# Optimization experiments

Hardware: AMD Instinct MI355X
Metric: run time of the kernel (lower is better)

## Reference

```python
import jax, jax.numpy as jnp
import numpy as np

HEADS1, HID, LSTM_H, OUT = 4, 64, 32, 2
NEG_SLOPE = 0.2
EPS = 1e-16


def gat_layer(x, src, dst, W, att_src, att_dst, bias, heads, out_ch):
    """PyG GATConv (concat=True, add_self_loops handled by caller)."""
    N = x.shape[0]
    h = (x @ W).reshape(N, heads, out_ch)                 # [N, H, C]
    a_s = jnp.sum(h * att_src, axis=-1)                    # [N, H]
    a_d = jnp.sum(h * att_dst, axis=-1)                    # [N, H]
    e = jax.nn.leaky_relu(a_s[src] + a_d[dst], NEG_SLOPE)  # [E, H]
    m = jax.ops.segment_max(e, dst, num_segments=N)        # scatter-softmax (stable)
    e = jnp.exp(e - jax.lax.stop_gradient(m)[dst])
    denom = jax.ops.segment_sum(e, dst, num_segments=N)
    alpha = e / (denom[dst] + EPS)                         # [E, H]
    msg = h[src] * alpha[..., None]                        # [E, H, C]
    out = jax.ops.segment_sum(msg, dst, num_segments=N)    # [N, H, C]
    return out.reshape(N, heads * out_ch) + bias


def lstm_last(seq, W_ih, W_hh, b_ih, b_hh, hidden):
    """Single-layer batch_first LSTM; returns last-step hidden state. Gate order i,f,g,o (torch)."""
    B = seq.shape[0]
    xT = jnp.transpose(seq, (1, 0, 2))  # [T, B, F]
    b = b_ih + b_hh

    def step(carry, xt):
        h, c = carry
        z = xt @ W_ih.T + h @ W_hh.T + b  # [B, 4H]
        i, f, g, o = jnp.split(z, 4, axis=-1)
        c = jax.nn.sigmoid(f) * c + jax.nn.sigmoid(i) * jnp.tanh(g)
        h = jax.nn.sigmoid(o) * jnp.tanh(c)
        return (h, c), None

    h0 = jnp.zeros((B, hidden), seq.dtype)
    (h, _), _ = jax.lax.scan(step, (h0, h0), xT)
    return h


def setup_inputs() -> dict:
    key = jax.random.key(0)
    ks = jax.random.split(key, 20)
    N, E, IN, T = 50000, 800000, 128, 50
    s = lambda k, shp: jax.random.normal(k, shp, jnp.float32) * 0.05
    inp = {
        "x": jax.random.normal(ks[0], (N, IN), jnp.float32),
        "edge_index": jax.random.randint(ks[1], (2, E), 0, N, jnp.int32),
        "sequences": jax.random.normal(ks[2], (N, T, 3), jnp.float32),
        # GATConv 1: in=128 -> 64 per head, 4 heads
        "W1": s(ks[3], (IN, HEADS1 * HID)),
        "att_src1": s(ks[4], (HEADS1, HID)),
        "att_dst1": s(ks[5], (HEADS1, HID)),
        "bias1": jnp.zeros((HEADS1 * HID,), jnp.float32),
        # GATConv 2: in=256 -> 64, 1 head
        "W2": s(ks[6], (HEADS1 * HID, HID)),
        "att_src2": s(ks[7], (1, HID)),
        "att_dst2": s(ks[8], (1, HID)),
        "bias2": jnp.zeros((HID,), jnp.float32),
        # LSTM(input_size=3, hidden_size=32)
        "W_ih": s(ks[9], (4 * LSTM_H, 3)),
        "W_hh": s(ks[10], (4 * LSTM_H, LSTM_H)),
        "b_ih": jnp.zeros((4 * LSTM_H,), jnp.float32),
        "b_hh": jnp.zeros((4 * LSTM_H,), jnp.float32),
        # fusion MLP: (64+32) -> 64 -> 2
        "Wf1": s(ks[11], (HID + LSTM_H, HID)),
        "bf1": jnp.zeros((HID,), jnp.float32),
        "Wf2": s(ks[12], (HID, OUT)),
        "bf2": jnp.zeros((OUT,), jnp.float32),
    }
    return inp


def reference(x, edge_index, sequences, W1, att_src1, att_dst1, bias1,
              W2, att_src2, att_dst2, bias2, W_ih, W_hh, b_ih, b_hh,
              Wf1, bf1, Wf2, bf2):
    N = x.shape[0]
    # PyG GATConv default add_self_loops=True
    loops = jnp.arange(N, dtype=edge_index.dtype)
    src = jnp.concatenate([edge_index[0], loops])
    dst = jnp.concatenate([edge_index[1], loops])

    g = jax.nn.elu(gat_layer(x, src, dst, W1, att_src1, att_dst1, bias1, HEADS1, HID))
    # dropout is identity in eval mode
    g = gat_layer(g, src, dst, W2, att_src2, att_dst2, bias2, 1, HID)  # [N, 64]

    t = lstm_last(sequences, W_ih, W_hh, b_ih, b_hh, LSTM_H)           # [N, 32]

    combined = jnp.concatenate([g, t], axis=1)
    h = jax.nn.relu(combined @ Wf1 + bf1)
    return h @ Wf2 + bf2
```

## Files before the change

### kernel.cpp

```cpp
#include <hip/hip_runtime.h>
#include <math.h>

#define HEADS1 4
#define HID 64
#define LSTM_H 32
#define IN_F 128
#define T_STEPS 50
#define NEG_SLOPE 0.2f
#define EPS_A 1e-16f

typedef __attribute__((ext_vector_type(8))) short short8;
typedef __attribute__((ext_vector_type(4))) float floatx4;
typedef __attribute__((ext_vector_type(4))) unsigned uint32x4;

__device__ __forceinline__ float frcp(float x) {
    float r;
    asm("v_rcp_f32 %0, %1" : "=v"(r) : "v"(x));
    return r;
}
__device__ __forceinline__ float sigf(float x) { return frcp(1.0f + __expf(-x)); }
__device__ __forceinline__ float tanhfast(float x) {
    float e = __expf(2.0f * x);
    return 1.0f - 2.0f * frcp(e + 1.0f);
}
__device__ __forceinline__ unsigned short f2bf(float f) {
    unsigned u = __float_as_uint(f);
    unsigned r = (u + 0x7FFFu + ((u >> 16) & 1u)) >> 16;
    return (unsigned short)r;
}
__device__ __forceinline__ float bf2f(unsigned short s) {
    return __uint_as_float(((unsigned)s) << 16);
}
__device__ __forceinline__ unsigned cvt_pk_bf16(float a, float b) {
    unsigned r;
    asm("v_cvt_pk_bf16_f32 %0, %1, %2" : "=v"(r) : "v"(a), "v"(b));
    return r;
}
__device__ __forceinline__ float lo16f(unsigned p) { return __uint_as_float(p << 16); }
__device__ __forceinline__ float hi16f(unsigned p) { return __uint_as_float(p & 0xffff0000u); }
__device__ __forceinline__ short8 bc8(uint32x4 v) { return __builtin_bit_cast(short8, v); }

template <int KK>
__global__ void prep_wt(const float* __restrict__ W, unsigned short* __restrict__ th,
                        unsigned short* __restrict__ tl, int total, int NC) {
    int i = blockIdx.x * 256 + threadIdx.x;
    if (i >= total) return;
    int n = i / KK, k = i - n * KK;
    float v = W[k * NC + n];
    unsigned short h = f2bf(v);
    th[i] = h;
    tl[i] = f2bf(v - bf2f(h));
}

template <int K, int NC>
__global__ __launch_bounds__(256)
void gemm_mfma(const float* __restrict__ A, const unsigned short* __restrict__ Bth,
               const unsigned short* __restrict__ Btl, float* __restrict__ C, int M) {
    __shared__ float sA[128][44];
    __shared__ unsigned short sBh[64][40];
    __shared__ unsigned short sBl[64][40];
    const int tid = threadIdx.x;
    const int wave = tid >> 6, lane = tid & 63;
    const int wr = wave >> 1, wc = wave & 1;
    const int row0 = blockIdx.x * 128;
    const int col0 = blockIdx.y * 64;
    const int l15 = lane & 15, l4 = lane >> 4;

    floatx4 acc[4][2];
#pragma unroll
    for (int rb = 0; rb < 4; rb++)
#pragma unroll
        for (int cb = 0; cb < 2; cb++) acc[rb][cb] = (floatx4){0.f, 0.f, 0.f, 0.f};

    for (int k0 = 0; k0 < K; k0 += 32) {
        __syncthreads();
#pragma unroll
        for (int q = 0; q < 4; q++) {
            int idx = q * 256 + tid;
            int row = idx >> 3, seg = idx & 7;
            int gr = row0 + row;
            float4 v = (gr < M) ? *(const float4*)&A[(size_t)gr * K + k0 + seg * 4]
                                : make_float4(0.f, 0.f, 0.f, 0.f);
            *(float4*)&sA[row][seg * 4] = v;
        }
        {
            int col = tid >> 2, seg = tid & 3;
            size_t gb = (size_t)(col0 + col) * K + k0 + seg * 8;
            *(short8*)&sBh[col][seg * 8] = *(const short8*)&Bth[gb];
            *(short8*)&sBl[col][seg * 8] = *(const short8*)&Btl[gb];
        }
        __syncthreads();

        short8 bh0 = *(const short8*)&sBh[wc * 32 + 0 + l15][l4 * 8];
        short8 bl0 = *(const short8*)&sBl[wc * 32 + 0 + l15][l4 * 8];
        short8 bh1 = *(const short8*)&sBh[wc * 32 + 16 + l15][l4 * 8];
        short8 bl1 = *(const short8*)&sBl[wc * 32 + 16 + l15][l4 * 8];

#pragma unroll
        for (int rb = 0; rb < 4; rb++) {
            int row = wr * 64 + rb * 16 + l15;
            floatx4 a0 = *(const floatx4*)&sA[row][l4 * 8 + 0];
            floatx4 a1 = *(const floatx4*)&sA[row][l4 * 8 + 4];
            unsigned p0 = cvt_pk_bf16(a0[0], a0[1]);
            unsigned p1 = cvt_pk_bf16(a0[2], a0[3]);
            unsigned p2 = cvt_pk_bf16(a1[0], a1[1]);
            unsigned p3 = cvt_pk_bf16(a1[2], a1[3]);
            uint32x4 hp = {p0, p1, p2, p3};
            short8 Ah = bc8(hp);
            unsigned q0 = cvt_pk_bf16(a0[0] - lo16f(p0), a0[1] - hi16f(p0));
            unsigned q1 = cvt_pk_bf16(a0[2] - lo16f(p1), a0[3] - hi16f(p1));
            unsigned q2 = cvt_pk_bf16(a1[0] - lo16f(p2), a1[1] - hi16f(p2));
            unsigned q3 = cvt_pk_bf16(a1[2] - lo16f(p3), a1[3] - hi16f(p3));
            uint32x4 lp = {q0, q1, q2, q3};
            short8 Al = bc8(lp);

            acc[rb][0] = __builtin_amdgcn_mfma_f32_16x16x32_bf16(Ah, bh0, acc[rb][0], 0, 0, 0);
            acc[rb][0] = __builtin_amdgcn_mfma_f32_16x16x32_bf16(Ah, bl0, acc[rb][0], 0, 0, 0);
            acc[rb][0] = __builtin_amdgcn_mfma_f32_16x16x32_bf16(Al, bh0, acc[rb][0], 0, 0, 0);
            acc[rb][1] = __builtin_amdgcn_mfma_f32_16x16x32_bf16(Ah, bh1, acc[rb][1], 0, 0, 0);
            acc[rb][1] = __builtin_amdgcn_mfma_f32_16x16x32_bf16(Ah, bl1, acc[rb][1], 0, 0, 0);
            acc[rb][1] = __builtin_amdgcn_mfma_f32_16x16x32_bf16(Al, bh1, acc[rb][1], 0, 0, 0);
        }
    }

#pragma unroll
    for (int rb = 0; rb < 4; rb++)
#pragma unroll
        for (int cb = 0; cb < 2; cb++)
#pragma unroll
            for (int q = 0; q < 4; q++) {
                int row = row0 + wr * 64 + rb * 16 + l4 * 4 + q;
                int col = col0 + wc * 32 + cb * 16 + l15;
                if (row < M) C[(size_t)row * NC + col] = acc[rb][cb][q];
            }
}

__global__ void att_scores(const float* __restrict__ h, const float* __restrict__ att_s,
                           const float* __restrict__ att_d, float* __restrict__ as_,
                           float* __restrict__ ad_, int NH, int Hmask) {
    int i = blockIdx.x * blockDim.x + threadIdx.x;
    if (i >= NH) return;
    int hh = i & Hmask;
    const float* row = h + (size_t)i * HID;
    float s = 0.0f, d = 0.0f;
#pragma unroll 8
    for (int c = 0; c < HID; c++) {
        float v = row[c];
        s += v * att_s[hh * HID + c];
        d += v * att_d[hh * HID + c];
    }
    as_[i] = s;
    ad_[i] = d;
}

__global__ void count_deg(const int* __restrict__ dsts, int E, int ET, int* __restrict__ cnt) {
    int e = blockIdx.x * blockDim.x + threadIdx.x;
    if (e >= ET) return;
    int d = (e < E) ? dsts[e] : (e - E);
    atomicAdd(&cnt[d], 1);
}

__global__ void scan1(const int* __restrict__ cnt, int* __restrict__ rowp,
                      int* __restrict__ bsum, int N) {
    __shared__ int tmp[256];
    int i = blockIdx.x * 256 + threadIdx.x;
    int v = (i < N) ? cnt[i] : 0;
    tmp[threadIdx.x] = v;
    __syncthreads();
    for (int off = 1; off < 256; off <<= 1) {
        int t = (threadIdx.x >= (unsigned)off) ? tmp[threadIdx.x - off] : 0;
        __syncthreads();
        tmp[threadIdx.x] += t;
        __syncthreads();
    }
    if (i < N) rowp[i] = tmp[threadIdx.x] - v;
    if (threadIdx.x == 255) bsum[blockIdx.x] = tmp[255];
}

__global__ void scan2(int* __restrict__ bsum, int nb) {
    __shared__ int tmp[256];
    int v = (threadIdx.x < (unsigned)nb) ? bsum[threadIdx.x] : 0;
    tmp[threadIdx.x] = v;
    __syncthreads();
    for (int off = 1; off < 256; off <<= 1) {
        int t = (threadIdx.x >= (unsigned)off) ? tmp[threadIdx.x - off] : 0;
        __syncthreads();
        tmp[threadIdx.x] += t;
        __syncthreads();
    }
    if (threadIdx.x < (unsigned)nb) bsum[threadIdx.x] = tmp[threadIdx.x] - v;
}

__global__ void scan3(int* __restrict__ rowp, const int* __restrict__ bsum, int N, int ET) {
    int i = blockIdx.x * 256 + threadIdx.x;
    if (i < N) rowp[i] += bsum[blockIdx.x];
    if (i == 0) rowp[N] = ET;
}

__global__ void scatter_edges(const int* __restrict__ dsts, int E, int ET,
                              const int* __restrict__ rowp, int* __restrict__ cursor,
                              int* __restrict__ eid) {
    int e = blockIdx.x * blockDim.x + threadIdx.x;
    if (e >= ET) return;
    int d = (e < E) ? dsts[e] : (e - E);
    int pos = atomicAdd(&cursor[d], 1);
    eid[rowp[d] + pos] = e;
}

__global__ __launch_bounds__(256)
void gat_agg4_sp(const int* __restrict__ srcs, int E,
                 const int* __restrict__ rowp, const int* __restrict__ eid,
                 const float* __restrict__ as_, const float* __restrict__ ad_,
                 const float* __restrict__ hfeat, const float* __restrict__ bias,
                 float* __restrict__ g, int N) {
    __shared__ float s_alpha[4][64][4];
    const int wave = threadIdx.x >> 6;
    const int lane = threadIdx.x & 63;
    const int head = lane >> 4;
    const int dst = blockIdx.x * 4 + wave;
    if (dst >= N) return;
    const int start = rowp[dst], end = rowp[dst + 1];
    const float4 adv = ((const float4*)ad_)[dst];
    const float4* h4 = (const float4*)hfeat;

    float4 dsum = make_float4(0.f, 0.f, 0.f, 0.f);
    float4 acc  = make_float4(0.f, 0.f, 0.f, 0.f);

    for (int i0 = start; i0 < end; i0 += 64) {
        int cnt = min(64, end - i0);
        int i = i0 + lane;
        int s = 0;
        if (i < end) {
            int e = eid[i];
            s = (e < E) ? srcs[e] : (e - E);
            float4 a = ((const float4*)as_)[s];
            float tx, ex;
            tx = a.x + adv.x; tx = (tx > 0.f) ? tx : NEG_SLOPE * tx; ex = __expf(tx);
            dsum.x += ex; s_alpha[wave][lane][0] = ex;
            tx = a.y + adv.y; tx = (tx > 0.f) ? tx : NEG_SLOPE * tx; ex = __expf(tx);
            dsum.y += ex; s_alpha[wave][lane][1] = ex;
            tx = a.z + adv.z; tx = (tx > 0.f) ? tx : NEG_SLOPE * tx; ex = __expf(tx);
            dsum.z += ex; s_alpha[wave][lane][2] = ex;
            tx = a.w + adv.w; tx = (tx > 0.f) ? tx : NEG_SLOPE * tx; ex = __expf(tx);
            dsum.w += ex; s_alpha[wave][lane][3] = ex;
        }
        __builtin_amdgcn_wave_barrier();
#pragma unroll 4
        for (int k = 0; k < cnt; k++) {
            float a_k = s_alpha[wave][k][head];
            int   s_k = __shfl(s, k);
            float4 hv = h4[(size_t)s_k * 64 + lane];
            acc.x += a_k * hv.x; acc.y += a_k * hv.y;
            acc.z += a_k * hv.z; acc.w += a_k * hv.w;
        }
        __builtin_amdgcn_wave_barrier();
    }
#pragma unroll
    for (int mk = 32; mk >= 1; mk >>= 1) {
        dsum.x += __shfl_xor(dsum.x, mk);
        dsum.y += __shfl_xor(dsum.y, mk);
        dsum.z += __shfl_xor(dsum.z, mk);
        dsum.w += __shfl_xor(dsum.w, mk);
    }
    float den = (head == 0) ? dsum.x : (head == 1) ? dsum.y : (head == 2) ? dsum.z : dsum.w;
    float inv = 1.0f / (den + EPS_A);
    float4 b4 = ((const float4*)bias)[lane];
    float4 r;
    r.x = acc.x * inv + b4.x; r.x = (r.x > 0.f) ? r.x : __expf(r.x) - 1.f;
    r.y = acc.y * inv + b4.y; r.y = (r.y > 0.f) ? r.y : __expf(r.y) - 1.f;
    r.z = acc.z * inv + b4.z; r.z = (r.z > 0.f) ? r.z : __expf(r.z) - 1.f;
    r.w = acc.w * inv + b4.w; r.w = (r.w > 0.f) ? r.w : __expf(r.w) - 1.f;
    ((float4*)g)[(size_t)dst * 64 + lane] = r;
}

__global__ __launch_bounds__(256)
void gat_agg1_sp(const int* __restrict__ srcs, int E,
                 const int* __restrict__ rowp, const int* __restrict__ eid,
                 const float* __restrict__ as_, const float* __restrict__ ad_,
                 const float* __restrict__ hfeat, const float* __restrict__ bias,
                 float* __restrict__ g, int N) {
    __shared__ float s_alpha[4][64];
    const int wave = threadIdx.x >> 6;
    const int lane = threadIdx.x & 63;
    const int dst = blockIdx.x * 4 + wave;
    if (dst >= N) return;
    const int start = rowp[dst], end = rowp[dst + 1];
    const float adv = ad_[dst];

    float dsum = 0.0f, acc = 0.0f;
    for (int i0 = start; i0 < end; i0 += 64) {
        int cnt = min(64, end - i0);
        int i = i0 + lane;
        int s = 0;
        if (i < end) {
            int e = eid[i];
            s = (e < E) ? srcs[e] : (e - E);
            float t = as_[s] + adv;
            t = (t > 0.f) ? t : NEG_SLOPE * t;
            float ex = __expf(t);
            dsum += ex;
            s_alpha[wave][lane] = ex;
        }
        __builtin_amdgcn_wave_barrier();
#pragma unroll 4
        for (int k = 0; k < cnt; k++) {
            float a_k = s_alpha[wave][k];
            int   s_k = __shfl(s, k);
            acc += a_k * hfeat[(size_t)s_k * 64 + lane];
        }
        __builtin_amdgcn_wave_barrier();
    }
#pragma unroll
    for (int mk = 32; mk >= 1; mk >>= 1) dsum += __shfl_xor(dsum, mk);
    g[(size_t)dst * 64 + lane] = acc / (dsum + EPS_A) + bias[lane];
}

__global__ void prep_wsplit(const float* __restrict__ Wih, const float* __restrict__ Whh,
                            const float* __restrict__ bih, const float* __restrict__ bhh,
                            uint32x4* __restrict__ wsp) {
    const int tid = threadIdx.x;
    const int kk = tid >> 7, sub = (tid >> 6) & 1, lane = tid & 63;
    const int grp = lane >> 4, col = lane & 15;
    const int krow = grp * 8;
    const int n = (sub + kk * 2) * 16 + col;
    float w[8];
    *(float4*)&w[0] = *(const float4*)&Whh[n * 32 + krow + 0];
    *(float4*)&w[4] = *(const float4*)&Whh[n * 32 + krow + 4];
    unsigned hi[8], lo[8];
#pragma unroll
    for (int j = 0; j < 8; j++) {
        unsigned short hs = f2bf(w[j]);
        hi[j] = hs;
        lo[j] = f2bf(w[j] - bf2f(hs));
    }
    uint32x4 BH = {hi[0] | (hi[1] << 16), hi[2] | (hi[3] << 16),
                   hi[4] | (hi[5] << 16), hi[6] | (hi[7] << 16)};
    uint32x4 BL = {lo[0] | (lo[1] << 16), lo[2] | (lo[3] << 16),
                   lo[4] | (lo[5] << 16), lo[6] | (lo[7] << 16)};
    float wi0 = Wih[n * 3 + 0], wi1 = Wih[n * 3 + 1], wi2 = Wih[n * 3 + 2];
    float bb = bih[n] + bhh[n];
    unsigned h0 = f2bf(wi0), h1 = f2bf(wi1), h2 = f2bf(wi2), hb = f2bf(bb);
    uint32x4 B2 = {0u, 0u, 0u, 0u};
    if (grp == 0) {
        unsigned bl_ = f2bf(bb - bf2f((unsigned short)hb));
        B2[0] = h0 | (h1 << 16); B2[1] = h2 | (hb << 16);
        B2[2] = h0 | (h1 << 16); B2[3] = h2 | (bl_ << 16);
    } else if (grp == 1) {
        unsigned l0 = f2bf(wi0 - bf2f((unsigned short)h0));
        unsigned l1 = f2bf(wi1 - bf2f((unsigned short)h1));
        unsigned l2 = f2bf(wi2 - bf2f((unsigned short)h2));
        B2[0] = l0 | (l1 << 16); B2[1] = l2;
    }
    wsp[((kk * 3 + 0) * 2 + sub) * 64 + lane] = B2;
    wsp[((kk * 3 + 1) * 2 + sub) * 64 + lane] = BH;
    wsp[((kk * 3 + 2) * 2 + sub) * 64 + lane] = BL;
}

__global__ __launch_bounds__(256)
void lstm_mfma(const float* __restrict__ seq, const uint32x4* __restrict__ wsp,
               float* __restrict__ t_out, int N) {
    __shared__ float s_h[2][2][16][36];

    const int tid  = threadIdx.x;
    const int wave = tid >> 6, lane = tid & 63;
    const int pair = wave >> 1, sub = wave & 1;
    const int grp  = lane >> 4, col = lane & 15;
    const int node0 = blockIdx.x * 32 + pair * 16;

#define LF(KK, W) wsp[(((KK) * 3 + (W)) * 2 + sub) * 64 + lane]
    uint32x4 B2_0 = LF(0, 0), BH_0 = LF(0, 1), BL_0 = LF(0, 2);
    uint32x4 B2_1 = LF(1, 0), BH_1 = LF(1, 1), BL_1 = LF(1, 2);
    uint32x4 B2_2 = LF(2, 0), BH_2 = LF(2, 1), BL_2 = LF(2, 2);
    uint32x4 B2_3 = LF(3, 0), BH_3 = LF(3, 1), BL_3 = LF(3, 2);
#undef LF
    asm volatile("" : "+v"(B2_0), "+v"(BH_0), "+v"(BL_0),
                      "+v"(B2_1), "+v"(BH_1), "+v"(BL_1),
                      "+v"(B2_2), "+v"(BH_2), "+v"(BL_2),
                      "+v"(B2_3), "+v"(BH_3), "+v"(BL_3));

    for (int i = tid; i < 2 * 2 * 16 * 36; i += 256) ((float*)s_h)[i] = 0.0f;
    __syncthreads();

    float cst0 = 0.f, cst1 = 0.f, cst2 = 0.f, cst3 = 0.f;
    float hn0 = 0.f, hn1 = 0.f, hn2 = 0.f, hn3 = 0.f;
    const floatx4 zac = {0.f, 0.f, 0.f, 0.f};

    const int nodeX = node0 + col;
    const bool vx = (nodeX < N) && (grp < 2);
    const bool g0 = (grp == 0);
    const float* xp = seq + (size_t)nodeX * (T_STEPS * 3);

    float xv0 = vx ? xp[0] : 0.0f;
    float xv1 = vx ? xp[1] : 0.0f;
    float xv2 = vx ? xp[2] : 0.0f;

#pragma unroll 1
    for (int t = 0; t < T_STEPS; t++) {
        unsigned w0 = cvt_pk_bf16(xv0, xv1);
        unsigned w1 = cvt_pk_bf16(xv2, g0 ? 1.0f : 0.0f);
        float e0 = xv0 - lo16f(w0);
        float e1 = xv1 - hi16f(w0);
        float e2 = xv2 - lo16f(w1);
        unsigned w2 = g0 ? cvt_pk_bf16(e0, e1) : 0u;
        unsigned w3 = g0 ? cvt_pk_bf16(e2, 1.0f) : 0u;
        uint32x4 a2p = {w0, w1, w2, w3};
        short8 A2 = bc8(a2p);

        const float* hr = &s_h[pair][(t + 1) & 1][col][grp * 8];
        floatx4 h0 = *(const floatx4*)&hr[0];
        floatx4 h1 = *(const floatx4*)&hr[4];
        unsigned p0 = cvt_pk_bf16(h0[0], h0[1]);
        unsigned p1 = cvt_pk_bf16(h0[2], h0[3]);
        unsigned p2 = cvt_pk_bf16(h1[0], h1[1]);
        unsigned p3 = cvt_pk_bf16(h1[2], h1[3]);
        uint32x4 hip = {p0, p1, p2, p3};
        short8 Ahi = bc8(hip);
        unsigned q0 = cvt_pk_bf16(h0[0] - lo16f(p0), h0[1] - hi16f(p0));
        unsigned q1 = cvt_pk_bf16(h0[2] - lo16f(p1), h0[3] - hi16f(p1));
        unsigned q2 = cvt_pk_bf16(h1[0] - lo16f(p2), h1[1] - hi16f(p2));
        unsigned q3 = cvt_pk_bf16(h1[2] - lo16f(p3), h1[3] - hi16f(p3));
        uint32x4 lop = {q0, q1, q2, q3};
        short8 Alo = bc8(lop);

        {
            int tn = (t + 1 < T_STEPS) ? (t + 1) : t;
            xv0 = vx ? xp[tn * 3 + 0] : 0.0f;
            xv1 = vx ? xp[tn * 3 + 1] : 0.0f;
            xv2 = vx ? xp[tn * 3 + 2] : 0.0f;
        }

        floatx4 d0 = __builtin_amdgcn_mfma_f32_16x16x32_bf16(A2, bc8(B2_0), zac, 0, 0, 0);
        d0 = __builtin_amdgcn_mfma_f32_16x16x32_bf16(Alo, bc8(BH_0), d0, 0, 0, 0);
        d0 = __builtin_amdgcn_mfma_f32_16x16x32_bf16(Ahi, bc8(BL_0), d0, 0, 0, 0);
        d0 = __builtin_amdgcn_mfma_f32_16x16x32_bf16(Ahi, bc8(BH_0), d0, 0, 0, 0);
        floatx4 d1 = __builtin_amdgcn_mfma_f32_16x16x32_bf16(A2, bc8(B2_1), zac, 0, 0, 0);
        d1 = __builtin_amdgcn_mfma_f32_16x16x32_bf16(Alo, bc8(BH_1), d1, 0, 0, 0);
        d1 = __builtin_amdgcn_mfma_f32_16x16x32_bf16(Ahi, bc8(BL_1), d1, 0, 0, 0);
        d1 = __builtin_amdgcn_mfma_f32_16x16x32_bf16(Ahi, bc8(BH_1), d1, 0, 0, 0);
        floatx4 d2 = __builtin_amdgcn_mfma_f32_16x16x32_bf16(A2, bc8(B2_2), zac, 0, 0, 0);
        d2 = __builtin_amdgcn_mfma_f32_16x16x32_bf16(Alo, bc8(BH_2), d2, 0, 0, 0);
        d2 = __builtin_amdgcn_mfma_f32_16x16x32_bf16(Ahi, bc8(BL_2), d2, 0, 0, 0);
        d2 = __builtin_amdgcn_mfma_f32_16x16x32_bf16(Ahi, bc8(BH_2), d2, 0, 0, 0);
        floatx4 d3 = __builtin_amdgcn_mfma_f32_16x16x32_bf16(A2, bc8(B2_3), zac, 0, 0, 0);
        d3 = __builtin_amdgcn_mfma_f32_16x16x32_bf16(Alo, bc8(BH_3), d3, 0, 0, 0);
        d3 = __builtin_amdgcn_mfma_f32_16x16x32_bf16(Ahi, bc8(BL_3), d3, 0, 0, 0);
        d3 = __builtin_amdgcn_mfma_f32_16x16x32_bf16(Ahi, bc8(BH_3), d3, 0, 0, 0);

        {
            float ig, fg, gv, og;
            ig = sigf(d0[0]); fg = sigf(d1[0]); gv = tanhfast(d2[0]); og = sigf(d3[0]);
            cst0 = fg * cst0 + ig * gv; hn0 = og * tanhfast(cst0);
            ig = sigf(d0[1]); fg = sigf(d1[1]); gv = tanhfast(d2[1]); og = sigf(d3[1]);
            cst1 = fg * cst1 + ig * gv; hn1 = og * tanhfast(cst1);
            ig = sigf(d0[2]); fg = sigf(d1[2]); gv = tanhfast(d2[2]); og = sigf(d3[2]);
            cst2 = fg * cst2 + ig * gv; hn2 = og * tanhfast(cst2);
            ig = sigf(d0[3]); fg = sigf(d1[3]); gv = tanhfast(d2[3]); og = sigf(d3[3]);
            cst3 = fg * cst3 + ig * gv; hn3 = og * tanhfast(cst3);
        }

        float* hw = &s_h[pair][t & 1][4 * grp][sub * 16 + col];
        hw[0 * 36] = hn0; hw[1 * 36] = hn1; hw[2 * 36] = hn2; hw[3 * 36] = hn3;
        __syncthreads();
    }

    {
        int node = node0 + 4 * grp;
        const int c = sub * 16 + col;
        if (node + 0 < N) t_out[(size_t)(node + 0) * LSTM_H + c] = hn0;
        if (node + 1 < N) t_out[(size_t)(node + 1) * LSTM_H + c] = hn1;
        if (node + 2 < N) t_out[(size_t)(node + 2) * LSTM_H + c] = hn2;
        if (node + 3 < N) t_out[(size_t)(node + 3) * LSTM_H + c] = hn3;
    }
}

__global__ void fusion_kernel(const float* __restrict__ g2, const float* __restrict__ tt,
                              const float* __restrict__ Wf1, const float* __restrict__ bf1,
                              const float* __restrict__ Wf2, const float* __restrict__ bf2,
                              float* __restrict__ out, int N) {
    __shared__ float sW[96 * 64];
    __shared__ float sb1[64];
    __shared__ float sW2[128];
    for (int i = threadIdx.x; i < 96 * 64; i += 256) sW[i] = Wf1[i];
    if (threadIdx.x < 64) sb1[threadIdx.x] = bf1[threadIdx.x];
    if (threadIdx.x < 128) sW2[threadIdx.x] = Wf2[threadIdx.x];
    __syncthreads();
    const int wave = threadIdx.x >> 6;
    const int lane = threadIdx.x & 63;
    for (int n = blockIdx.x * 4 + wave; n < N; n += gridDim.x * 4) {
        const float* gn = g2 + (size_t)n * 64;
        const float* tn = tt + (size_t)n * 32;
        float acc = sb1[lane];
#pragma unroll 8
        for (int k = 0; k < 64; k++) acc += gn[k] * sW[k * 64 + lane];
#pragma unroll 8
        for (int k = 0; k < 32; k++) acc += tn[k] * sW[(64 + k) * 64 + lane];
        acc = fmaxf(acc, 0.0f);
        float o0 = acc * sW2[lane * 2 + 0];
        float o1 = acc * sW2[lane * 2 + 1];
#pragma unroll
    for (int mk = 32; mk >= 1; mk >>= 1) {
            o0 += __shfl_xor(o0, mk);
            o1 += __shfl_xor(o1, mk);
        }
        if (lane == 0) {
            out[(size_t)n * 2 + 0] = o0 + bf2[0];
            out[(size_t)n * 2 + 1] = o1 + bf2[1];
        }
    }
}

extern "C" void kernel_launch(void* const* d_in, const int* in_sizes, int n_in,
                              void* d_out, int out_size, void* d_ws, size_t ws_size,
                              hipStream_t stream) {
    const float* x      = (const float*)d_in[0];
    const int*   eidx   = (const int*)d_in[1];
    const float* seq    = (const float*)d_in[2];
    const float* W1     = (const float*)d_in[3];
    const float* att_s1 = (const float*)d_in[4];
    const float* att_d1 = (const float*)d_in[5];
    const float* bias1  = (const float*)d_in[6];
    const float* W2     = (const float*)d_in[7];
    const float* att_s2 = (const float*)d_in[8];
    const float* att_d2 = (const float*)d_in[9];
    const float* bias2  = (const float*)d_in[10];
    const float* Wih    = (const float*)d_in[11];
    const float* Whh    = (const float*)d_in[12];
    const float* bih    = (const float*)d_in[13];
    const float* bhh    = (const float*)d_in[14];
    const float* Wf1    = (const float*)d_in[15];
    const float* bf1    = (const float*)d_in[16];
    const float* Wf2    = (const float*)d_in[17];
    const float* bf2    = (const float*)d_in[18];
    float* out = (float*)d_out;

    const int N  = in_sizes[0] / IN_F;
    const int E  = in_sizes[1] / 2;
    const int ET = E + N;
    const int* srcs = eidx;
    const int* dsts = eidx + E;

    float* fws = (float*)d_ws;
    size_t o = 0;
    float* h1  = fws + o; o += (size_t)N * 256;
    float* g1  = fws + o; o += (size_t)N * 256;
    float* as1 = fws + o; o += (size_t)N * 4;
    float* ad1 = fws + o; o += (size_t)N * 4;
    int* cnt    = (int*)(fws + o);
    int* rowp   = cnt + N;
    int* cursor = rowp + N + 1;
    int* eid    = cursor + N;
    int* bsum   = eid + ET;
    uintptr_t wp_ = (uintptr_t)(bsum + 512);
    wp_ = (wp_ + 15) & ~(uintptr_t)15;
    uint32x4* wsp = (uint32x4*)wp_;
    unsigned short* w1h = (unsigned short*)(wsp + 1536);
    unsigned short* w1l = w1h + 32768;
    unsigned short* w2h = w1l + 32768;
    unsigned short* w2l = w2h + 16384;
    float* h2 = h1;
    float* g2 = h1 + (size_t)N * 64;
    float* tt = h1 + (size_t)N * 128;
    float* as2 = as1; float* ad2 = ad1;

    const int nTiles = (N + 255) / 256;
    dim3 blk(256);

    hipMemsetAsync(cnt, 0, (size_t)N * sizeof(int), stream);
    hipMemsetAsync(cursor, 0, (size_t)N * sizeof(int), stream);
    count_deg<<<(ET + 255) / 256, blk, 0, stream>>>(dsts, E, ET, cnt);
    scan1<<<nTiles, blk, 0, stream>>>(cnt, rowp, bsum, N);
    scan2<<<1, blk, 0, stream>>>(bsum, nTiles);
    scan3<<<(N + 256) / 256, blk, 0, stream>>>(rowp, bsum, N, ET);
    scatter_edges<<<(ET + 255) / 256, blk, 0, stream>>>(dsts, E, ET, rowp, cursor, eid);

    prep_wsplit<<<1, 512, 0, stream>>>(Wih, Whh, bih, bhh, wsp);
    prep_wt<128><<<(32768 + 255) / 256, blk, 0, stream>>>(W1, w1h, w1l, 32768, 256);
    prep_wt<256><<<(16384 + 255) / 256, blk, 0, stream>>>(W2, w2h, w2l, 16384, 64);

    gemm_mfma<128, 256><<<dim3((N + 127) / 128, 4), blk, 0, stream>>>(x, w1h, w1l, h1, N);
    att_scores<<<(N * 4 + 255) / 256, blk, 0, stream>>>(h1, att_s1, att_d1, as1, ad1, N * 4, 3);
    gat_agg4_sp<<<(N + 3) / 4, blk, 0, stream>>>(srcs, E, rowp, eid, as1, ad1, h1, bias1, g1, N);

    lstm_mfma<<<(N + 31) / 32, dim3(256), 0, stream>>>(seq, wsp, tt, N);

    gemm_mfma<256, 64><<<dim3((N + 127) / 128, 1), blk, 0, stream>>>(g1, w2h, w2l, h2, N);
    att_scores<<<(N + 255) / 256, blk, 0, stream>>>(h2, att_s2, att_d2, as2, ad2, N, 0);
    gat_agg1_sp<<<(N + 3) / 4, blk, 0, stream>>>(srcs, E, rowp, eid, as2, ad2, h2, bias2, g2, N);

    fusion_kernel<<<512, blk, 0, stream>>>(g2, tt, Wf1, bf1, Wf2, bf2, out, N);
}
```

Baseline: 728.5 us.

## Merge layer-1 GAT aggregation and LSTM into one interleaved kernel launch

Combines the 4-head GAT aggregation kernel and the MFMA LSTM kernel into a single launch, interleaving one LSTM block per nine blocks so that latency-bound LSTM work overlaps with memory-bound gather work. The LSTM output buffer moves to a dedicated workspace region so it no longer aliases h1, which the aggregation still reads. Shared memory becomes a union sized for the larger user, which may lower occupancy for aggregation blocks and adds per-block branching.

```diff
diff --git a/kernel.cpp b/kernel.cpp
--- a/kernel.cpp
+++ b/kernel.cpp
@@ -205,72 +205,6 @@
     int d = (e < E) ? dsts[e] : (e - E);
     int pos = atomicAdd(&cursor[d], 1);
     eid[rowp[d] + pos] = e;
-}
-
-__global__ __launch_bounds__(256)
-void gat_agg4_sp(const int* __restrict__ srcs, int E,
-                 const int* __restrict__ rowp, const int* __restrict__ eid,
-                 const float* __restrict__ as_, const float* __restrict__ ad_,
-                 const float* __restrict__ hfeat, const float* __restrict__ bias,
-                 float* __restrict__ g, int N) {
-    __shared__ float s_alpha[4][64][4];
-    const int wave = threadIdx.x >> 6;
-    const int lane = threadIdx.x & 63;
-    const int head = lane >> 4;
-    const int dst = blockIdx.x * 4 + wave;
-    if (dst >= N) return;
-    const int start = rowp[dst], end = rowp[dst + 1];
-    const float4 adv = ((const float4*)ad_)[dst];
-    const float4* h4 = (const float4*)hfeat;
-
-    float4 dsum = make_float4(0.f, 0.f, 0.f, 0.f);
-    float4 acc  = make_float4(0.f, 0.f, 0.f, 0.f);
-
-    for (int i0 = start; i0 < end; i0 += 64) {
-        int cnt = min(64, end - i0);
-        int i = i0 + lane;
-        int s = 0;
-        if (i < end) {
-            int e = eid[i];
-            s = (e < E) ? srcs[e] : (e - E);
-            float4 a = ((const float4*)as_)[s];
-            float tx, ex;
-            tx = a.x + adv.x; tx = (tx > 0.f) ? tx : NEG_SLOPE * tx; ex = __expf(tx);
-            dsum.x += ex; s_alpha[wave][lane][0] = ex;
-            tx = a.y + adv.y; tx = (tx > 0.f) ? tx : NEG_SLOPE * tx; ex = __expf(tx);
-            dsum.y += ex; s_alpha[wave][lane][1] = ex;
-            tx = a.z + adv.z; tx = (tx > 0.f) ? tx : NEG_SLOPE * tx; ex = __expf(tx);
-            dsum.z += ex; s_alpha[wave][lane][2] = ex;
-            tx = a.w + adv.w; tx = (tx > 0.f) ? tx : NEG_SLOPE * tx; ex = __expf(tx);
-            dsum.w += ex; s_alpha[wave][lane][3] = ex;
-        }
-        __builtin_amdgcn_wave_barrier();
-#pragma unroll 4
-        for (int k = 0; k < cnt; k++) {
-            float a_k = s_alpha[wave][k][head];
-            int   s_k = __shfl(s, k);
-            float4 hv = h4[(size_t)s_k * 64 + lane];
-            acc.x += a_k * hv.x; acc.y += a_k * hv.y;
-            acc.z += a_k * hv.z; acc.w += a_k * hv.w;
-        }
-        __builtin_amdgcn_wave_barrier();
-    }
-#pragma unroll
-    for (int mk = 32; mk >= 1; mk >>= 1) {
-        dsum.x += __shfl_xor(dsum.x, mk);
-        dsum.y += __shfl_xor(dsum.y, mk);
-        dsum.z += __shfl_xor(dsum.z, mk);
-        dsum.w += __shfl_xor(dsum.w, mk);
-    }
-    float den = (head == 0) ? dsum.x : (head == 1) ? dsum.y : (head == 2) ? dsum.z : dsum.w;
-    float inv = 1.0f / (den + EPS_A);
-    float4 b4 = ((const float4*)bias)[lane];
-    float4 r;
-    r.x = acc.x * inv + b4.x; r.x = (r.x > 0.f) ? r.x : __expf(r.x) - 1.f;
-    r.y = acc.y * inv + b4.y; r.y = (r.y > 0.f) ? r.y : __expf(r.y) - 1.f;
-    r.z = acc.z * inv + b4.z; r.z = (r.z > 0.f) ? r.z : __expf(r.z) - 1.f;
-    r.w = acc.w * inv + b4.w; r.w = (r.w > 0.f) ? r.w : __expf(r.w) - 1.f;
-    ((float4*)g)[(size_t)dst * 64 + lane] = r;
 }
 
 __global__ __launch_bounds__(256)
@@ -357,119 +291,194 @@
 }
 
 __global__ __launch_bounds__(256)
-void lstm_mfma(const float* __restrict__ seq, const uint32x4* __restrict__ wsp,
-               float* __restrict__ t_out, int N) {
-    __shared__ float s_h[2][2][16][36];
-
-    const int tid  = threadIdx.x;
-    const int wave = tid >> 6, lane = tid & 63;
-    const int pair = wave >> 1, sub = wave & 1;
-    const int grp  = lane >> 4, col = lane & 15;
-    const int node0 = blockIdx.x * 32 + pair * 16;
+void agg4_lstm(const int* __restrict__ srcs, int E,
+               const int* __restrict__ rowp, const int* __restrict__ eid,
+               const float* __restrict__ as_, const float* __restrict__ ad_,
+               const float* __restrict__ hfeat, const float* __restrict__ bias,
+               float* __restrict__ g,
+               const float* __restrict__ seq, const uint32x4* __restrict__ wsp,
+               float* __restrict__ t_out, int N, int nLstm) {
+    __shared__ float smem[2304];
+
+    const int bid = blockIdx.x;
+    const bool isLstm = (bid % 9 == 0) && (bid / 9 < nLstm);
+
+    if (isLstm) {
+        float (*s_h)[2][16][36] = (float(*)[2][16][36])smem;
+        const int lbid = bid / 9;
+        const int tid  = threadIdx.x;
+        const int wave = tid >> 6, lane = tid & 63;
+        const int pair = wave >> 1, sub = wave & 1;
+        const int grp  = lane >> 4, col = lane & 15;
+        const int node0 = lbid * 32 + pair * 16;
 
 #define LF(KK, W) wsp[(((KK) * 3 + (W)) * 2 + sub) * 64 + lane]
-    uint32x4 B2_0 = LF(0, 0), BH_0 = LF(0, 1), BL_0 = LF(0, 2);
-    uint32x4 B2_1 = LF(1, 0), BH_1 = LF(1, 1), BL_1 = LF(1, 2);
-    uint32x4 B2_2 = LF(2, 0), BH_2 = LF(2, 1), BL_2 = LF(2, 2);
-    uint32x4 B2_3 = LF(3, 0), BH_3 = LF(3, 1), BL_3 = LF(3, 2);
+        uint32x4 B2_0 = LF(0, 0), BH_0 = LF(0, 1), BL_0 = LF(0, 2);
+        uint32x4 B2_1 = LF(1, 0), BH_1 = LF(1, 1), BL_1 = LF(1, 2);
+        uint32x4 B2_2 = LF(2, 0), BH_2 = LF(2, 1), BL_2 = LF(2, 2);
+        uint32x4 B2_3 = LF(3, 0), BH_3 = LF(3, 1), BL_3 = LF(3, 2);
 #undef LF
-    asm volatile("" : "+v"(B2_0), "+v"(BH_0), "+v"(BL_0),
-                      "+v"(B2_1), "+v"(BH_1), "+v"(BL_1),
-                      "+v"(B2_2), "+v"(BH_2), "+v"(BL_2),
-                      "+v"(B2_3), "+v"(BH_3), "+v"(BL_3));
-
-    for (int i = tid; i < 2 * 2 * 16 * 36; i += 256) ((float*)s_h)[i] = 0.0f;
-    __syncthreads();
-
-    float cst0 = 0.f, cst1 = 0.f, cst2 = 0.f, cst3 = 0.f;
-    float hn0 = 0.f, hn1 = 0.f, hn2 = 0.f, hn3 = 0.f;
-    const floatx4 zac = {0.f, 0.f, 0.f, 0.f};
-
-    const int nodeX = node0 + col;
-    const bool vx = (nodeX < N) && (grp < 2);
-    const bool g0 = (grp == 0);
-    const float* xp = seq + (size_t)nodeX * (T_STEPS * 3);
-
-    float xv0 = vx ? xp[0] : 0.0f;
-    float xv1 = vx ? xp[1] : 0.0f;
-    float xv2 = vx ? xp[2] : 0.0f;
+        asm volatile("" : "+v"(B2_0), "+v"(BH_0), "+v"(BL_0),
+                          "+v"(B2_1), "+v"(BH_1), "+v"(BL_1),
+                          "+v"(B2_2), "+v"(BH_2), "+v"(BL_2),
+                          "+v"(B2_3), "+v"(BH_3), "+v"(BL_3));
+
+        for (int i = tid; i < 2 * 2 * 16 * 36; i += 256) smem[i] = 0.0f;
+        __syncthreads();
+
+        float cst0 = 0.f, cst1 = 0.f, cst2 = 0.f, cst3 = 0.f;
+        float hn0 = 0.f, hn1 = 0.f, hn2 = 0.f, hn3 = 0.f;
+        const floatx4 zac = {0.f, 0.f, 0.f, 0.f};
+
+        const int nodeX = node0 + col;
+        const bool vx = (nodeX < N) && (grp < 2);
+        const bool g0 = (grp == 0);
+        const float* xp = seq + (size_t)nodeX * (T_STEPS * 3);
+
+        float xv0 = vx ? xp[0] : 0.0f;
+        float xv1 = vx ? xp[1] : 0.0f;
+        float xv2 = vx ? xp[2] : 0.0f;
 
 #pragma unroll 1
-    for (int t = 0; t < T_STEPS; t++) {
-        unsigned w0 = cvt_pk_bf16(xv0, xv1);
-        unsigned w1 = cvt_pk_bf16(xv2, g0 ? 1.0f : 0.0f);
-        float e0 = xv0 - lo16f(w0);
-        float e1 = xv1 - hi16f(w0);
-        float e2 = xv2 - lo16f(w1);
-        unsigned w2 = g0 ? cvt_pk_bf16(e0, e1) : 0u;
-        unsigned w3 = g0 ? cvt_pk_bf16(e2, 1.0f) : 0u;
-        uint32x4 a2p = {w0, w1, w2, w3};
-        short8 A2 = bc8(a2p);
-
-        const float* hr = &s_h[pair][(t + 1) & 1][col][grp * 8];
-        floatx4 h0 = *(const floatx4*)&hr[0];
-        floatx4 h1 = *(const floatx4*)&hr[4];
-        unsigned p0 = cvt_pk_bf16(h0[0], h0[1]);
-        unsigned p1 = cvt_pk_bf16(h0[2], h0[3]);
-        unsigned p2 = cvt_pk_bf16(h1[0], h1[1]);
-        unsigned p3 = cvt_pk_bf16(h1[2], h1[3]);
-        uint32x4 hip = {p0, p1, p2, p3};
-        short8 Ahi = bc8(hip);
-        unsigned q0 = cvt_pk_bf16(h0[0] - lo16f(p0), h0[1] - hi16f(p0));
-        unsigned q1 = cvt_pk_bf16(h0[2] - lo16f(p1), h0[3] - hi16f(p1));
-        unsigned q2 = cvt_pk_bf16(h1[0] - lo16f(p2), h1[1] - hi16f(p2));
-        unsigned q3 = cvt_pk_bf16(h1[2] - lo16f(p3), h1[3] - hi16f(p3));
-        uint32x4 lop = {q0, q1, q2, q3};
-        short8 Alo = bc8(lop);
+        for (int t = 0; t < T_STEPS; t++) {
+            unsigned w0 = cvt_pk_bf16(xv0, xv1);
+            unsigned w1 = cvt_pk_bf16(xv2, g0 ? 1.0f : 0.0f);
+            float e0 = xv0 - lo16f(w0);
+            float e1 = xv1 - hi16f(w0);
+            float e2 = xv2 - lo16f(w1);
+            unsigned w2 = g0 ? cvt_pk_bf16(e0, e1) : 0u;
+            unsigned w3 = g0 ? cvt_pk_bf16(e2, 1.0f) : 0u;
+            uint32x4 a2p = {w0, w1, w2, w3};
+            short8 A2 = bc8(a2p);
+
+            const float* hr = &s_h[pair][(t + 1) & 1][col][grp * 8];
+            floatx4 h0 = *(const floatx4*)&hr[0];
+            floatx4 h1 = *(const floatx4*)&hr[4];
+            unsigned p0 = cvt_pk_bf16(h0[0], h0[1]);
+            unsigned p1 = cvt_pk_bf16(h0[2], h0[3]);
+            unsigned p2 = cvt_pk_bf16(h1[0], h1[1]);
+            unsigned p3 = cvt_pk_bf16(h1[2], h1[3]);
+            uint32x4 hip = {p0, p1, p2, p3};
+            short8 Ahi = bc8(hip);
+            unsigned q0 = cvt_pk_bf16(h0[0] - lo16f(p0), h0[1] - hi16f(p0));
+            unsigned q1 = cvt_pk_bf16(h0[2] - lo16f(p1), h0[3] - hi16f(p1));
+            unsigned q2 = cvt_pk_bf16(h1[0] - lo16f(p2), h1[1] - hi16f(p2));
+            unsigned q3 = cvt_pk_bf16(h1[2] - lo16f(p3), h1[3] - hi16f(p3));
+            uint32x4 lop = {q0, q1, q2, q3};
+            short8 Alo = bc8(lop);
+
+            {
+                int tn = (t + 1 < T_STEPS) ? (t + 1) : t;
+                xv0 = vx ? xp[tn * 3 + 0] : 0.0f;
+                xv1 = vx ? xp[tn * 3 + 1] : 0.0f;
+                xv2 = vx ? xp[tn * 3 + 2] : 0.0f;
+            }
+
+            floatx4 d0 = __builtin_amdgcn_mfma_f32_16x16x32_bf16(A2, bc8(B2_0), zac, 0, 0, 0);
+            d0 = __builtin_amdgcn_mfma_f32_16x16x32_bf16(Alo, bc8(BH_0), d0, 0, 0, 0);
+            d0 = __builtin_amdgcn_mfma_f32_16x16x32_bf16(Ahi, bc8(BL_0), d0, 0, 0, 0);
+            d0 = __builtin_amdgcn_mfma_f32_16x16x32_bf16(Ahi, bc8(BH_0), d0, 0, 0, 0);
+            floatx4 d1 = __builtin_amdgcn_mfma_f32_16x16x32_bf16(A2, bc8(B2_1), zac, 0, 0, 0);
+            d1 = __builtin_amdgcn_mfma_f32_16x16x32_bf16(Alo, bc8(BH_1), d1, 0, 0, 0);
+            d1 = __builtin_amdgcn_mfma_f32_16x16x32_bf16(Ahi, bc8(BL_1), d1, 0, 0, 0);
+            d1 = __builtin_amdgcn_mfma_f32_16x16x32_bf16(Ahi, bc8(BH_1), d1, 0, 0, 0);
+            floatx4 d2 = __builtin_amdgcn_mfma_f32_16x16x32_bf16(A2, bc8(B2_2), zac, 0, 0, 0);
+            d2 = __builtin_amdgcn_mfma_f32_16x16x32_bf16(Alo, bc8(BH_2), d2, 0, 0, 0);
+            d2 = __builtin_amdgcn_mfma_f32_16x16x32_bf16(Ahi, bc8(BL_2), d2, 0, 0, 0);
+            d2 = __builtin_amdgcn_mfma_f32_16x16x32_bf16(Ahi, bc8(BH_2), d2, 0, 0, 0);
+            floatx4 d3 = __builtin_amdgcn_mfma_f32_16x16x32_bf16(A2, bc8(B2_3), zac, 0, 0, 0);
+            d3 = __builtin_amdgcn_mfma_f32_16x16x32_bf16(Alo, bc8(BH_3), d3, 0, 0, 0);
+            d3 = __builtin_amdgcn_mfma_f32_16x16x32_bf16(Ahi, bc8(BL_3), d3, 0, 0, 0);
+            d3 = __builtin_amdgcn_mfma_f32_16x16x32_bf16(Ahi, bc8(BH_3), d3, 0, 0, 0);
+
+            {
+                float ig, fg, gv, og;
+                ig = sigf(d0[0]); fg = sigf(d1[0]); gv = tanhfast(d2[0]); og = sigf(d3[0]);
+                cst0 = fg * cst0 + ig * gv; hn0 = og * tanhfast(cst0);
+                ig = sigf(d0[1]); fg = sigf(d1[1]); gv = tanhfast(d2[1]); og = sigf(d3[1]);
+                cst1 = fg * cst1 + ig * gv; hn1 = og * tanhfast(cst1);
+                ig = sigf(d0[2]); fg = sigf(d1[2]); gv = tanhfast(d2[2]); og = sigf(d3[2]);
+                cst2 = fg * cst2 + ig * gv; hn2 = og * tanhfast(cst2);
+                ig = sigf(d0[3]); fg = sigf(d1[3]); gv = tanhfast(d2[3]); og = sigf(d3[3]);
+                cst3 = fg * cst3 + ig * gv; hn3 = og * tanhfast(cst3);
+            }
+
+            float* hw = &s_h[pair][t & 1][4 * grp][sub * 16 + col];
+            hw[0 * 36] = hn0; hw[1 * 36] = hn1; hw[2 * 36] = hn2; hw[3 * 36] = hn3;
+            __syncthreads();
+        }
 
         {
-            int tn = (t + 1 < T_STEPS) ? (t + 1) : t;
-            xv0 = vx ? xp[tn * 3 + 0] : 0.0f;
-            xv1 = vx ? xp[tn * 3 + 1] : 0.0f;
-            xv2 = vx ? xp[tn * 3 + 2] : 0.0f;
-        }
-
-        floatx4 d0 = __builtin_amdgcn_mfma_f32_16x16x32_bf16(A2, bc8(B2_0), zac, 0, 0, 0);
-        d0 = __builtin_amdgcn_mfma_f32_16x16x32_bf16(Alo, bc8(BH_0), d0, 0, 0, 0);
-        d0 = __builtin_amdgcn_mfma_f32_16x16x32_bf16(Ahi, bc8(BL_0), d0, 0, 0, 0);
-        d0 = __builtin_amdgcn_mfma_f32_16x16x32_bf16(Ahi, bc8(BH_0), d0, 0, 0, 0);
-        floatx4 d1 = __builtin_amdgcn_mfma_f32_16x16x32_bf16(A2, bc8(B2_1), zac, 0, 0, 0);
-        d1 = __builtin_amdgcn_mfma_f32_16x16x32_bf16(Alo, bc8(BH_1), d1, 0, 0, 0);
-        d1 = __builtin_amdgcn_mfma_f32_16x16x32_bf16(Ahi, bc8(BL_1), d1, 0, 0, 0);
-        d1 = __builtin_amdgcn_mfma_f32_16x16x32_bf16(Ahi, bc8(BH_1), d1, 0, 0, 0);
-        floatx4 d2 = __builtin_amdgcn_mfma_f32_16x16x32_bf16(A2, bc8(B2_2), zac, 0, 0, 0);
-        d2 = __builtin_amdgcn_mfma_f32_16x16x32_bf16(Alo, bc8(BH_2), d2, 0, 0, 0);
-        d2 = __builtin_amdgcn_mfma_f32_16x16x32_bf16(Ahi, bc8(BL_2), d2, 0, 0, 0);
-        d2 = __builtin_amdgcn_mfma_f32_16x16x32_bf16(Ahi, bc8(BH_2), d2, 0, 0, 0);
-        floatx4 d3 = __builtin_amdgcn_mfma_f32_16x16x32_bf16(A2, bc8(B2_3), zac, 0, 0, 0);
-        d3 = __builtin_amdgcn_mfma_f32_16x16x32_bf16(Alo, bc8(BH_3), d3, 0, 0, 0);
-        d3 = __builtin_amdgcn_mfma_f32_16x16x32_bf16(Ahi, bc8(BL_3), d3, 0, 0, 0);
-        d3 = __builtin_amdgcn_mfma_f32_16x16x32_bf16(Ahi, bc8(BH_3), d3, 0, 0, 0);
-
-        {
-            float ig, fg, gv, og;
-            ig = sigf(d0[0]); fg = sigf(d1[0]); gv = tanhfast(d2[0]); og = sigf(d3[0]);
-            cst0 = fg * cst0 + ig * gv; hn0 = og * tanhfast(cst0);
-            ig = sigf(d0[1]); fg = sigf(d1[1]); gv = tanhfast(d2[1]); og = sigf(d3[1]);
-            cst1 = fg * cst1 + ig * gv; hn1 = og * tanhfast(cst1);
-            ig = sigf(d0[2]); fg = sigf(d1[2]); gv = tanhfast(d2[2]); og = sigf(d3[2]);
-            cst2 = fg * cst2 + ig * gv; hn2 = og * tanhfast(cst2);
-            ig = sigf(d0[3]); fg = sigf(d1[3]); gv = tanhfast(d2[3]); og = sigf(d3[3]);
-            cst3 = fg * cst3 + ig * gv; hn3 = og * tanhfast(cst3);
-        }
-
-        float* hw = &s_h[pair][t & 1][4 * grp][sub * 16 + col];
-        hw[0 * 36] = hn0; hw[1 * 36] = hn1; hw[2 * 36] = hn2; hw[3 * 36] = hn3;
-        __syncthreads();
+            int node = node0 + 4 * grp;
+            const int c = sub * 16 + col;
+            if (node + 0 < N) t_out[(size_t)(node + 0) * LSTM_H + c] = hn0;
+            if (node + 1 < N) t_out[(size_t)(node + 1) * LSTM_H + c] = hn1;
+            if (node + 2 < N) t_out[(size_t)(node + 2) * LSTM_H + c] = hn2;
+            if (node + 3 < N) t_out[(size_t)(node + 3) * LSTM_H + c] = hn3;
+        }
+        return;
     }
 
     {
-        int node = node0 + 4 * grp;
-        const int c = sub * 16 + col;
-        if (node + 0 < N) t_out[(size_t)(node + 0) * LSTM_H + c] = hn0;
-        if (node + 1 < N) t_out[(size_t)(node + 1) * LSTM_H + c] = hn1;
-        if (node + 2 < N) t_out[(size_t)(node + 2) * LSTM_H + c] = hn2;
-        if (node + 3 < N) t_out[(size_t)(node + 3) * LSTM_H + c] = hn3;
+        float (*s_alpha)[64][4] = (float(*)[64][4])smem;
+        const int aid = bid - bid / 9 - 1;
+        const int wave = threadIdx.x >> 6;
+        const int lane = threadIdx.x & 63;
+        const int head = lane >> 4;
+        const int dst = aid * 4 + wave;
+        if (dst >= N) return;
+        const int start = rowp[dst], end = rowp[dst + 1];
+        const float4 adv = ((const float4*)ad_)[dst];
+        const float4* h4 = (const float4*)hfeat;
+
+        float4 dsum = make_float4(0.f, 0.f, 0.f, 0.f);
+        float4 acc  = make_float4(0.f, 0.f, 0.f, 0.f);
+
+        for (int i0 = start; i0 < end; i0 += 64) {
+            int cnt = min(64, end - i0);
+            int i = i0 + lane;
+            int s = 0;
+            if (i < end) {
+                int e = eid[i];
+                s = (e < E) ? srcs[e] : (e - E);
+                float4 a = ((const float4*)as_)[s];
+                float tx, ex;
+                tx = a.x + adv.x; tx = (tx > 0.f) ? tx : NEG_SLOPE * tx; ex = __expf(tx);
+                dsum.x += ex; s_alpha[wave][lane][0] = ex;
+                tx = a.y + adv.y; tx = (tx > 0.f) ? tx : NEG_SLOPE * tx; ex = __expf(tx);
+                dsum.y += ex; s_alpha[wave][lane][1] = ex;
+                tx = a.z + adv.z; tx = (tx > 0.f) ? tx : NEG_SLOPE * tx; ex = __expf(tx);
+                dsum.z += ex; s_alpha[wave][lane][2] = ex;
+                tx = a.w + adv.w; tx = (tx > 0.f) ? tx : NEG_SLOPE * tx; ex = __expf(tx);
+                dsum.w += ex; s_alpha[wave][lane][3] = ex;
+            }
+            __builtin_amdgcn_wave_barrier();
+#pragma unroll 4
+            for (int k = 0; k < cnt; k++) {
+                float a_k = s_alpha[wave][k][head];
+                int   s_k = __shfl(s, k);
+                float4 hv = h4[(size_t)s_k * 64 + lane];
+                acc.x += a_k * hv.x; acc.y += a_k * hv.y;
+                acc.z += a_k * hv.z; acc.w += a_k * hv.w;
+            }
+            __builtin_amdgcn_wave_barrier();
+        }
+#pragma unroll
+        for (int mk = 32; mk >= 1; mk >>= 1) {
+            dsum.x += __shfl_xor(dsum.x, mk);
+            dsum.y += __shfl_xor(dsum.y, mk);
+            dsum.z += __shfl_xor(dsum.z, mk);
+            dsum.w += __shfl_xor(dsum.w, mk);
+        }
+        float den = (head == 0) ? dsum.x : (head == 1) ? dsum.y : (head == 2) ? dsum.z : dsum.w;
+        float inv = 1.0f / (den + EPS_A);
+        float4 b4 = ((const float4*)bias)[lane];
+        float4 r;
+        r.x = acc.x * inv + b4.x; r.x = (r.x > 0.f) ? r.x : __expf(r.x) - 1.f;
+        r.y = acc.y * inv + b4.y; r.y = (r.y > 0.f) ? r.y : __expf(r.y) - 1.f;
+        r.z = acc.z * inv + b4.z; r.z = (r.z > 0.f) ? r.z : __expf(r.z) - 1.f;
+        r.w = acc.w * inv + b4.w; r.w = (r.w > 0.f) ? r.w : __expf(r.w) - 1.f;
+        ((float4*)g)[(size_t)dst * 64 + lane] = r;
     }
 }
 
@@ -498,7 +507,7 @@
         float o0 = acc * sW2[lane * 2 + 0];
         float o1 = acc * sW2[lane * 2 + 1];
 #pragma unroll
-    for (int mk = 32; mk >= 1; mk >>= 1) {
+        for (int mk = 32; mk >= 1; mk >>= 1) {
             o0 += __shfl_xor(o0, mk);
             o1 += __shfl_xor(o1, mk);
         }
@@ -543,6 +552,7 @@
     size_t o = 0;
     float* h1  = fws + o; o += (size_t)N * 256;
     float* g1  = fws + o; o += (size_t)N * 256;
+    float* tt  = fws + o; o += (size_t)N * 32;
     float* as1 = fws + o; o += (size_t)N * 4;
     float* ad1 = fws + o; o += (size_t)N * 4;
     int* cnt    = (int*)(fws + o);
@@ -559,7 +569,6 @@
     unsigned short* w2l = w2h + 16384;
     float* h2 = h1;
     float* g2 = h1 + (size_t)N * 64;
-    float* tt = h1 + (size_t)N * 128;
     float* as2 = as1; float* ad2 = ad1;
 
     const int nTiles = (N + 255) / 256;
@@ -579,9 +588,13 @@
 
     gemm_mfma<128, 256><<<dim3((N + 127) / 128, 4), blk, 0, stream>>>(x, w1h, w1l, h1, N);
     att_scores<<<(N * 4 + 255) / 256, blk, 0, stream>>>(h1, att_s1, att_d1, as1, ad1, N * 4, 3);
-    gat_agg4_sp<<<(N + 3) / 4, blk, 0, stream>>>(srcs, E, rowp, eid, as1, ad1, h1, bias1, g1, N);
-
-    lstm_mfma<<<(N + 31) / 32, dim3(256), 0, stream>>>(seq, wsp, tt, N);
+
+    {
+        const int nLstm = (N + 31) / 32;
+        const int nAgg  = (N + 3) / 4;
+        agg4_lstm<<<nLstm + nAgg, blk, 0, stream>>>(srcs, E, rowp, eid, as1, ad1,
+                                                    h1, bias1, g1, seq, wsp, tt, N, nLstm);
+    }
 
     gemm_mfma<256, 64><<<dim3((N + 127) / 128, 1), blk, 0, stream>>>(g1, w2h, w2l, h2, N);
     att_scores<<<(N + 255) / 256, blk, 0, stream>>>(h2, att_s2, att_d2, as2, ad2, N, 0);
```

After: 699.3 us. -4.0%, faster.
